# Kernel tuning notes

Hardware: AMD Instinct MI355X
Metric: run time of the kernel (lower is better)

The kernel has to match this reference:

```python
import jax, jax.numpy as jnp
import numpy as np

N_NODES = 100000
N_EDGES = 1600000
HID = 128
MAX_Z = 1000
N_GRAPHS = 1000
N_LAYERS = 3


def setup_inputs() -> dict:
    key = jax.random.key(0)
    ks = jax.random.split(key, 10)
    z = jax.random.randint(ks[0], (N_NODES,), 0, MAX_Z)
    edge_index = jax.random.randint(ks[1], (2, N_EDGES), 0, N_NODES)
    batch = jnp.sort(jax.random.randint(ks[2], (N_NODES,), 0, N_GRAPHS))
    s = 1.0 / np.sqrt(HID)
    z_emb = jax.random.normal(ks[3], (MAX_Z, HID), jnp.float32)
    Wl = jax.random.normal(ks[4], (N_LAYERS, HID, HID), jnp.float32) * s
    bl = jnp.zeros((N_LAYERS, HID), jnp.float32)
    Wr = jax.random.normal(ks[5], (N_LAYERS, HID, HID), jnp.float32) * s
    lin1_w = jax.random.normal(ks[6], (HID, HID), jnp.float32) * s
    lin1_b = jnp.zeros((HID,), jnp.float32)
    lin2_w = jax.random.normal(ks[7], (1, HID), jnp.float32) * s
    lin2_b = jnp.zeros((1,), jnp.float32)
    return dict(z=z, edge_index=edge_index, batch=batch, num_graphs=N_GRAPHS,
                z_emb=z_emb, Wl=Wl, bl=bl, Wr=Wr,
                lin1_w=lin1_w, lin1_b=lin1_b, lin2_w=lin2_w, lin2_b=lin2_b)


def _sage_conv(x, src, dst, deg_inv, Wl_i, bl_i, Wr_i):
    # PyG SAGEConv (default): out = lin_l(mean_{j in N(i)} x_j) + lin_r(x_i)
    agg = jax.ops.segment_sum(x[src], dst, num_segments=x.shape[0]) * deg_inv[:, None]
    return agg @ Wl_i.T + bl_i + x @ Wr_i.T


def reference(z, edge_index, batch, num_graphs, z_emb, Wl, bl, Wr, lin1_w, lin1_b, lin2_w, lin2_b):
    x = z_emb[z]  # z.ndim == 1 -> z_emb.ndim == 2, no sum branch
    src, dst = edge_index[0], edge_index[1]
    n = x.shape[0]
    deg = jax.ops.segment_sum(jnp.ones((src.shape[0],), x.dtype), dst, num_segments=n)
    deg_inv = 1.0 / jnp.maximum(deg, 1.0)  # mean aggregation; empty neighborhoods -> 0
    for i in range(Wl.shape[0] - 1):
        x = jax.nn.relu(_sage_conv(x, src, dst, deg_inv, Wl[i], bl[i], Wr[i]))
        # dropout is identity in eval mode
    x = _sage_conv(x, src, dst, deg_inv, Wl[-1], bl[-1], Wr[-1])
    # batch is sorted; first occurrence of each graph id == searchsorted
    center = jnp.searchsorted(batch, jnp.arange(num_graphs))
    h = x[center] * x[center + 1]
    h = jax.nn.relu(h @ lin1_w.T + lin1_b)
    return h @ lin2_w.T + lin2_b  # [num_graphs, 1]
```

## Files before the change

### kernel.cpp

```cpp
#include <hip/hip_runtime.h>
#include <hip/hip_bf16.h>
#include <cstdint>

#define HID 128
#define GM 128
#define SCAN_CHUNK 2048
#define NBIN 512
#define CHUNK 2048
#define MAXHI 1024

typedef __attribute__((ext_vector_type(8))) short bf16x8;
typedef __attribute__((ext_vector_type(4))) float f32x4;

__device__ __forceinline__ unsigned short f2bf(float f) {
    union { __hip_bfloat16 h; unsigned short u; } c;
    c.h = __float2bfloat16(f);
    return c.u;
}
__device__ __forceinline__ float bf2f(unsigned short u) {
    union { unsigned int i; float f; } c;
    c.i = ((unsigned int)u) << 16;
    return c.f;
}
__device__ __forceinline__ unsigned int pack2(unsigned short a, unsigned short b) {
    return (unsigned int)a | ((unsigned int)b << 16);
}
__device__ __forceinline__ bf16x8 ld_frag(const unsigned int* p) {
    union { uint4 u; bf16x8 f; } c;
    c.u = *(const uint4*)p;
    return c.f;
}

__device__ __forceinline__ int block_scan_excl(int v, int t, int* wtot, int* tot) {
    int lane = t & 63, wv = t >> 6;
    int incl = v;
#pragma unroll
    for (int off = 1; off < 64; off <<= 1) {
        int u = __shfl_up(incl, off);
        if (lane >= off) incl += u;
    }
    if (lane == 63) wtot[wv] = incl;
    __syncthreads();
    int woff = 0;
    for (int w = 0; w < wv; ++w) woff += wtot[w];
    if (tot) *tot = wtot[0] + wtot[1] + wtot[2] + wtot[3];
    __syncthreads();
    return woff + incl - v;
}

__global__ __launch_bounds__(256) void k_hist(const int* __restrict__ dst,
                                              int* __restrict__ hist, int n_edges) {
    __shared__ int h[NBIN];
    int t = threadIdx.x;
    h[t] = 0; h[t + 256] = 0;
    __syncthreads();
    int base = blockIdx.x * CHUNK;
#pragma unroll
    for (int j = 0; j < CHUNK / 256; ++j) {
        int e = base + j * 256 + t;
        if (e < n_edges) atomicAdd(&h[dst[e] & (NBIN - 1)], 1);
    }
    __syncthreads();
    hist[(size_t)blockIdx.x * NBIN + t] = h[t];
    hist[(size_t)blockIdx.x * NBIN + t + 256] = h[t + 256];
}

__global__ __launch_bounds__(256) void k_colscan(int* __restrict__ hist,
                                                 int* __restrict__ bintotal, int B) {
    __shared__ int wtot[4];
    int k = blockIdx.x, t = threadIdx.x;
    int run = 0;
    for (int base = 0; base < B; base += 256) {
        int b = base + t;
        int v = (b < B) ? hist[(size_t)b * NBIN + k] : 0;
        int tot;
        int excl = block_scan_excl(v, t, wtot, &tot);
        if (b < B) hist[(size_t)b * NBIN + k] = run + excl;
        run += tot;
    }
    if (t == 0) bintotal[k] = run;
}

__global__ __launch_bounds__(256) void k_binbase(const int* __restrict__ bintotal,
                                                 int* __restrict__ binbase) {
    __shared__ int wtot[4];
    int t = threadIdx.x;
    int a0 = bintotal[2 * t], a1 = bintotal[2 * t + 1];
    int excl = block_scan_excl(a0 + a1, t, wtot, nullptr);
    binbase[2 * t] = excl;
    binbase[2 * t + 1] = excl + a0;
    if (t == 255) binbase[NBIN] = excl + a0 + a1;
}

__global__ __launch_bounds__(256) void k_route(const int* __restrict__ src,
                                               const int* __restrict__ dst,
                                               const int* __restrict__ histex,
                                               const int* __restrict__ binbase,
                                               int2* __restrict__ ebuf, int n_edges) {
    __shared__ int h2[NBIN];
    __shared__ int basel[NBIN];
    int t = threadIdx.x;
    h2[t] = 0; h2[t + 256] = 0;
    basel[t]       = binbase[t]       + histex[(size_t)blockIdx.x * NBIN + t];
    basel[t + 256] = binbase[t + 256] + histex[(size_t)blockIdx.x * NBIN + t + 256];
    __syncthreads();
    int base = blockIdx.x * CHUNK;
#pragma unroll
    for (int j = 0; j < CHUNK / 256; ++j) {
        int e = base + j * 256 + t;
        if (e < n_edges) {
            int d = dst[e], s = src[e];
            int bin = d & (NBIN - 1);
            int r = atomicAdd(&h2[bin], 1);
            ebuf[basel[bin] + r] = make_int2(s, d);
        }
    }
}

__global__ __launch_bounds__(256) void k_group(const int2* __restrict__ ebuf,
                                               const int* __restrict__ binbase,
                                               const int* __restrict__ z,
                                               int* __restrict__ csr_src,
                                               int* __restrict__ csr_zoff,
                                               int* __restrict__ start, int* __restrict__ deg,
                                               int n_nodes) {
    __shared__ int hh[MAXHI];
    __shared__ int cur[MAXHI];
    __shared__ int wtot[4];
    int k = blockIdx.x, t = threadIdx.x;
    int rs = binbase[k], re = binbase[k + 1];
#pragma unroll
    for (int j = 0; j < MAXHI / 256; ++j) hh[t + j * 256] = 0;
    __syncthreads();
    for (int i = rs + t; i < re; i += 256)
        atomicAdd(&hh[ebuf[i].y >> 9], 1);
    __syncthreads();
    int idx = t * 4;
    int a0 = hh[idx], a1 = hh[idx + 1], a2 = hh[idx + 2], a3 = hh[idx + 3];
    int excl = block_scan_excl(a0 + a1 + a2 + a3, t, wtot, nullptr);
    int e0 = excl, e1 = e0 + a0, e2 = e1 + a1, e3 = e2 + a2;
    cur[idx] = e0; cur[idx + 1] = e1; cur[idx + 2] = e2; cur[idx + 3] = e3;
    int ee[4] = {e0, e1, e2, e3};
    int aa[4] = {a0, a1, a2, a3};
#pragma unroll
    for (int j = 0; j < 4; ++j) {
        int node = ((idx + j) << 9) | k;
        if (node < n_nodes) {
            start[node] = rs + ee[j];
            deg[node] = aa[j];
        }
    }
    __syncthreads();
    for (int i = rs + t; i < re; i += 256) {
        int2 sd = ebuf[i];
        int r = rs + atomicAdd(&cur[sd.y >> 9], 1);
        csr_src[r] = sd.x;
        csr_zoff[r] = z[sd.x] << 9;
    }
}

__global__ void k_scan1(const int* __restrict__ v_in, int* __restrict__ partials, int n) {
    __shared__ int sm[256];
    int t = threadIdx.x;
    int base = blockIdx.x * SCAN_CHUNK + t * 8;
    int s = 0;
#pragma unroll
    for (int j = 0; j < 8; ++j) { int i = base + j; if (i < n) s += v_in[i]; }
    sm[t] = s;
    __syncthreads();
    for (int off = 128; off > 0; off >>= 1) {
        if (t < off) sm[t] += sm[t + off];
        __syncthreads();
    }
    if (t == 0) partials[blockIdx.x] = sm[0];
}

__global__ void k_scan2(int* partials, int nchunks, int* total) {
    int lane = threadIdx.x;
    int v = (lane < nchunks) ? partials[lane] : 0;
#pragma unroll
    for (int off = 1; off < 64; off <<= 1) {
        int u = __shfl_up(v, off);
        if (lane >= off) v += u;
    }
    if (total && lane == nchunks - 1) *total = v;
    int ex = __shfl_up(v, 1);
    if (lane == 0) ex = 0;
    if (lane < nchunks) partials[lane] = ex;
}

__global__ void k_compact(const int* __restrict__ flag, const int* __restrict__ partials,
                          int* __restrict__ remap, int* __restrict__ nodes2, int n) {
    __shared__ int wtot[4];
    int t = threadIdx.x;
    int lane = t & 63, wv = t >> 6;
    int base = blockIdx.x * SCAN_CHUNK + t * 8;
    int v[8];
    int ts = 0;
#pragma unroll
    for (int j = 0; j < 8; ++j) { int i = base + j; v[j] = (i < n) ? flag[i] : 0; ts += v[j]; }
    int incl = ts;
#pragma unroll
    for (int off = 1; off < 64; off <<= 1) {
        int u = __shfl_up(incl, off);
        if (lane >= off) incl += u;
    }
    if (lane == 63) wtot[wv] = incl;
    __syncthreads();
    int woff = 0;
    for (int w = 0; w < wv; ++w) woff += wtot[w];
    int run = partials[blockIdx.x] + woff + (incl - ts);
#pragma unroll
    for (int j = 0; j < 8; ++j) {
        int i = base + j;
        if (i < n) {
            remap[i] = run;
            if (v[j]) nodes2[run] = i;
        }
        run += v[j];
    }
}

__global__ void k_prep(const float* __restrict__ z_emb, const float* __restrict__ Wl,
                       const float* __restrict__ Wr, const float* __restrict__ bl,
                       float* __restrict__ zl, float* __restrict__ zr,
                       unsigned short* __restrict__ wh, unsigned short* __restrict__ wlo,
                       int max_z) {
    int t = threadIdx.x;
    if ((int)blockIdx.x < max_z) {
        __shared__ float row[HID];
        int r = blockIdx.x;
        if (t < HID) row[t] = z_emb[(size_t)r * HID + t];
        __syncthreads();
        int d = t & 127;
        const float* w = (t < 128 ? Wl : Wr) + (size_t)d * HID;
        float acc = 0.f;
#pragma unroll
        for (int k4 = 0; k4 < HID / 4; ++k4) {
            float4 wv = *(const float4*)(w + k4 * 4);
            float4 hv = *(const float4*)&row[k4 * 4];
            acc += wv.x * hv.x + wv.y * hv.y + wv.z * hv.z + wv.w * hv.w;
        }
        if (t < 128) zl[(size_t)r * HID + d] = acc;
        else         zr[(size_t)r * HID + d] = acc + bl[d];
    } else {
        int idx = (blockIdx.x - max_z) * 256 + t;
        if (idx >= 3 * HID * 2 * HID) return;
        int l = idx / (HID * 2 * HID);
        int r = idx - l * (HID * 2 * HID);
        int d = r >> 8;
        int k = r & 255;
        float v = (k < HID) ? Wl[((size_t)l * HID + d) * HID + k]
                            : Wr[((size_t)l * HID + d) * HID + (k - HID)];
        unsigned short h = f2bf(v);
        unsigned short lo = f2bf(v - bf2f(h));
        wh[idx] = h;
        wlo[idx] = lo;
    }
}

__global__ void k_flag(const int* __restrict__ sel, const int* __restrict__ start,
                       const int* __restrict__ deg,
                       const int* __restrict__ csr_src, int* __restrict__ flag, int n_sel) {
    int r = (blockIdx.x * blockDim.x + threadIdx.x) >> 6;
    int lane = threadIdx.x & 63;
    if (r >= n_sel) return;
    int node = sel[r];
    if (lane == 0) flag[node] = 1;
    int s = start[node], e = s + deg[node];
    for (int i = s + lane; i < e; i += 64) flag[csr_src[i]] = 1;
}

template<int MODE>
__global__ __launch_bounds__(256) void k_agg(const float* __restrict__ xv_,
                      float* __restrict__ aggout,
                      const int* __restrict__ start, const int* __restrict__ deg,
                      const int* __restrict__ csr_src, const int* __restrict__ csr_zoff,
                      const int* __restrict__ idxmap, const int* __restrict__ remap,
                      const int* __restrict__ z, const float* __restrict__ zr,
                      int n_host, const int* __restrict__ n_dev) {
    int nw_total = gridDim.x * 4;
    int w0 = blockIdx.x * 4 + (threadIdx.x >> 6);
    int lane = threadIdx.x & 63;
    int n = n_dev ? *n_dev : n_host;
    int half = lane >> 5;
    int col = lane & 31;
    const float4* xv = (const float4*)xv_;
    const char* xc = (const char*)xv_;
    for (int r = w0; r < n; r += nw_total) {
        int node = (MODE == 1) ? r : idxmap[r];
        int s = start[node];
        int dg = deg[node];
        int e = s + dg;
        float4 a0 = {0.f,0.f,0.f,0.f};
        if (MODE == 1) {
            for (int i = s + half; i < e; i += 16) {
                int off[8];
                float msk[8];
#pragma unroll
                for (int k = 0; k < 8; ++k) {
                    int p = i + 2 * k;
                    bool valid = p < e;
                    off[k] = csr_zoff[valid ? p : e - 1];
                    msk[k] = valid ? 1.f : 0.f;
                }
                float4 v[8];
#pragma unroll
                for (int k = 0; k < 8; ++k)
                    v[k] = ((const float4*)(xc + off[k]))[col];
#pragma unroll
                for (int k = 0; k < 8; ++k) {
                    a0.x = fmaf(v[k].x, msk[k], a0.x);
                    a0.y = fmaf(v[k].y, msk[k], a0.y);
                    a0.z = fmaf(v[k].z, msk[k], a0.z);
                    a0.w = fmaf(v[k].w, msk[k], a0.w);
                }
            }
        } else {
            float4 a1 = {0.f,0.f,0.f,0.f}, a2 = {0.f,0.f,0.f,0.f}, a3 = {0.f,0.f,0.f,0.f};
            int i = s + half;
            for (; i + 6 < e; i += 8) {
                int s0 = csr_src[i];
                int s1 = csr_src[i + 2];
                int s2 = csr_src[i + 4];
                int s3 = csr_src[i + 6];
                if (MODE == 3) { s0 = remap[s0]; s1 = remap[s1]; s2 = remap[s2]; s3 = remap[s3]; }
                float4 v0 = xv[(size_t)s0 * 32 + col];
                float4 v1 = xv[(size_t)s1 * 32 + col];
                float4 v2 = xv[(size_t)s2 * 32 + col];
                float4 v3 = xv[(size_t)s3 * 32 + col];
                a0.x += v0.x; a0.y += v0.y; a0.z += v0.z; a0.w += v0.w;
                a1.x += v1.x; a1.y += v1.y; a1.z += v1.z; a1.w += v1.w;
                a2.x += v2.x; a2.y += v2.y; a2.z += v2.z; a2.w += v2.w;
                a3.x += v3.x; a3.y += v3.y; a3.z += v3.z; a3.w += v3.w;
            }
            for (; i < e; i += 2) {
                int s0 = csr_src[i];
                if (MODE == 3) s0 = remap[s0];
                float4 v0 = xv[(size_t)s0 * 32 + col];
                a0.x += v0.x; a0.y += v0.y; a0.z += v0.z; a0.w += v0.w;
            }
            a0.x += a1.x + a2.x + a3.x;
            a0.y += a1.y + a2.y + a3.y;
            a0.z += a1.z + a2.z + a3.z;
            a0.w += a1.w + a2.w + a3.w;
        }
        a0.x += __shfl_xor(a0.x, 32);
        a0.y += __shfl_xor(a0.y, 32);
        a0.z += __shfl_xor(a0.z, 32);
        a0.w += __shfl_xor(a0.w, 32);
        if (half == 0) {
            float di = 1.0f / fmaxf((float)dg, 1.0f);
            float4 o = make_float4(a0.x * di, a0.y * di, a0.z * di, a0.w * di);
            if (MODE == 1) {
                int zn = z[node];
                float4 rv = ((const float4*)zr)[(size_t)zn * 32 + col];
                o.x = fmaxf(o.x + rv.x, 0.f);
                o.y = fmaxf(o.y + rv.y, 0.f);
                o.z = fmaxf(o.z + rv.z, 0.f);
                o.w = fmaxf(o.w + rv.w, 0.f);
            }
            ((float4*)aggout)[(size_t)r * 32 + col] = o;
        }
    }
}

__global__ __launch_bounds__(256) void k_gemm(const float* __restrict__ aggsrc,
                                              const float* __restrict__ xsrc,
                                              float* __restrict__ out,
                                              const unsigned short* __restrict__ wh,
                                              const unsigned short* __restrict__ wlo,
                                              const float* __restrict__ bias,
                                              const int* __restrict__ xidx,
                                              const int* __restrict__ remap2,
                                              int n_host, const int* __restrict__ n_dev,
                                              int do_relu) {
    __shared__ unsigned int sAh[GM * 16], sAl[GM * 16];
    __shared__ unsigned int sBh[HID * 16], sBl[HID * 16];
    int n_rows = n_dev ? *n_dev : n_host;
    int t = threadIdx.x;
    int node0 = blockIdx.x * GM;
    if (node0 >= n_rows) return;
    int wv = t >> 6, lane = t & 63;
    int lrow = lane & 15, lk = lane >> 4;

    f32x4 acc[2][8];
#pragma unroll
    for (int m = 0; m < 2; ++m)
#pragma unroll
        for (int n = 0; n < 8; ++n) acc[m][n] = (f32x4){0.f, 0.f, 0.f, 0.f};

    int srow = t >> 2;
    int sq = t & 3;

    int gg[2] = {node0 + srow, node0 + srow + 64};
    bool vv[2] = {gg[0] < n_rows, gg[1] < n_rows};
    int xr[2];
#pragma unroll
    for (int rr = 0; rr < 2; ++rr) {
        int v = xidx ? (vv[rr] ? xidx[gg[rr]] : 0) : gg[rr];
        xr[rr] = remap2 ? remap2[v] : v;
    }

    for (int c = 0; c < 8; ++c) {
        int kbase = (c & 3) * 32;
        int kb = c * 32;
#pragma unroll
        for (int rr = 0; rr < 2; ++rr) {
            int row = srow + rr * 64;
            const float* srcrow = (c < 4) ? aggsrc + (size_t)gg[rr] * HID
                                          : xsrc + (size_t)xr[rr] * HID;
            float f[8];
            if (vv[rr]) {
                const float4* rp = (const float4*)(srcrow + kbase + sq * 8);
                float4 v0 = rp[0], v1 = rp[1];
                f[0]=v0.x; f[1]=v0.y; f[2]=v0.z; f[3]=v0.w;
                f[4]=v1.x; f[5]=v1.y; f[6]=v1.z; f[7]=v1.w;
            } else {
#pragma unroll
                for (int j = 0; j < 8; ++j) f[j] = 0.f;
            }
            unsigned int h[4], l[4];
#pragma unroll
            for (int j = 0; j < 4; ++j) {
                unsigned short h0 = f2bf(f[2*j]), h1 = f2bf(f[2*j+1]);
                unsigned short l0 = f2bf(f[2*j] - bf2f(h0));
                unsigned short l1 = f2bf(f[2*j+1] - bf2f(h1));
                h[j] = pack2(h0, h1);
                l[j] = pack2(l0, l1);
            }
            unsigned int base = row * 16 + sq * 4;
            *(uint4*)&sAh[base] = make_uint4(h[0], h[1], h[2], h[3]);
            *(uint4*)&sAl[base] = make_uint4(l[0], l[1], l[2], l[3]);
        }
#pragma unroll
        for (int rr = 0; rr < 2; ++rr) {
            int d = srow + rr * 64;
            size_t go = (size_t)d * 256 + kb + sq * 8;
            uint4 vh = *(const uint4*)(wh + go);
            uint4 vl = *(const uint4*)(wlo + go);
            unsigned int base = d * 16 + sq * 4;
            *(uint4*)&sBh[base] = vh;
            *(uint4*)&sBl[base] = vl;
        }
        __syncthreads();
        bf16x8 ah0, al0, ah1, al1;
        {
            unsigned int a0 = (unsigned)(wv * 32 + lrow) * 16 + lk * 4;
            unsigned int a1 = (unsigned)(wv * 32 + 16 + lrow) * 16 + lk * 4;
            ah0 = ld_frag(&sAh[a0]); al0 = ld_frag(&sAl[a0]);
            ah1 = ld_frag(&sAh[a1]); al1 = ld_frag(&sAl[a1]);
        }
#pragma unroll
        for (int n = 0; n < 8; ++n) {
            unsigned int b = (unsigned)(n * 16 + lrow) * 16 + lk * 4;
            bf16x8 bh = ld_frag(&sBh[b]);
            bf16x8 bl = ld_frag(&sBl[b]);
            acc[0][n] = __builtin_amdgcn_mfma_f32_16x16x32_bf16(ah0, bh, acc[0][n], 0, 0, 0);
            acc[0][n] = __builtin_amdgcn_mfma_f32_16x16x32_bf16(al0, bh, acc[0][n], 0, 0, 0);
            acc[0][n] = __builtin_amdgcn_mfma_f32_16x16x32_bf16(ah0, bl, acc[0][n], 0, 0, 0);
            acc[1][n] = __builtin_amdgcn_mfma_f32_16x16x32_bf16(ah1, bh, acc[1][n], 0, 0, 0);
            acc[1][n] = __builtin_amdgcn_mfma_f32_16x16x32_bf16(al1, bh, acc[1][n], 0, 0, 0);
            acc[1][n] = __builtin_amdgcn_mfma_f32_16x16x32_bf16(ah1, bl, acc[1][n], 0, 0, 0);
        }
        __syncthreads();
    }
#pragma unroll
    for (int m = 0; m < 2; ++m) {
        int rbase = node0 + wv * 32 + m * 16 + lk * 4;
#pragma unroll
        for (int n = 0; n < 8; ++n) {
            int colb = n * 16 + lrow;
            float bb = bias[colb];
#pragma unroll
            for (int r = 0; r < 4; ++r) {
                int row = rbase + r;
                if (row < n_rows) {
                    float v = acc[m][n][r] + bb;
                    if (do_relu) v = fmaxf(v, 0.f);
                    out[(size_t)row * HID + colb] = v;
                }
            }
        }
    }
}

__global__ void k_center(const int* __restrict__ batch, int* __restrict__ sel,
                         int n_nodes, int n_graphs) {
    int g = blockIdx.x * blockDim.x + threadIdx.x;
    if (g >= n_graphs) return;
    int lo = 0, hi = n_nodes;
    while (lo < hi) {
        int mid = (lo + hi) >> 1;
        if (batch[mid] < g) lo = mid + 1;
        else hi = mid;
    }
    sel[2 * g]     = min(lo, n_nodes - 1);
    sel[2 * g + 1] = min(lo + 1, n_nodes - 1);
}

__global__ void k_readout(const float* __restrict__ y,
                          const float* __restrict__ w1, const float* __restrict__ b1,
                          const float* __restrict__ w2, const float* __restrict__ b2,
                          float* __restrict__ out, int n_graphs) {
    __shared__ float h[HID];
    int g = blockIdx.x;
    if (g >= n_graphs) return;
    int lane = threadIdx.x;
    float2 a = ((const float2*)(y + (size_t)(2 * g) * HID))[lane];
    float2 b = ((const float2*)(y + (size_t)(2 * g + 1) * HID))[lane];
    h[2 * lane] = a.x * b.x;
    h[2 * lane + 1] = a.y * b.y;
    __syncthreads();
    int d0 = 2 * lane;
    float acc0 = b1[d0], acc1 = b1[d0 + 1];
    const float4* w1a = (const float4*)(w1 + (size_t)d0 * HID);
    const float4* w1b = (const float4*)(w1 + (size_t)(d0 + 1) * HID);
#pragma unroll 8
    for (int k4 = 0; k4 < HID / 4; ++k4) {
        float4 hv = *(const float4*)&h[k4 * 4];
        float4 wa = w1a[k4];
        float4 wb = w1b[k4];
        acc0 += hv.x * wa.x + hv.y * wa.y + hv.z * wa.z + hv.w * wa.w;
        acc1 += hv.x * wb.x + hv.y * wb.y + hv.z * wb.z + hv.w * wb.w;
    }
    float p = fmaxf(acc0, 0.f) * w2[d0] + fmaxf(acc1, 0.f) * w2[d0 + 1];
#pragma unroll
    for (int off = 32; off > 0; off >>= 1) p += __shfl_down(p, off);
    if (lane == 0) out[g] = p + b2[0];
}

extern "C" void kernel_launch(void* const* d_in, const int* in_sizes, int n_in,
                              void* d_out, int out_size, void* d_ws, size_t ws_size,
                              hipStream_t stream) {
    const int* z = (const int*)d_in[0];
    const int* edge_index = (const int*)d_in[1];
    const int* batch = (const int*)d_in[2];
    const float* z_emb = (const float*)d_in[4];
    const float* Wl = (const float*)d_in[5];
    const float* bl = (const float*)d_in[6];
    const float* Wr = (const float*)d_in[7];
    const float* lin1_w = (const float*)d_in[8];
    const float* lin1_b = (const float*)d_in[9];
    const float* lin2_w = (const float*)d_in[10];
    const float* lin2_b = (const float*)d_in[11];
    float* out = (float*)d_out;

    int n_nodes = in_sizes[0];
    int n_edges = in_sizes[1] / 2;
    int max_z = in_sizes[4] / HID;
    int n_graphs = out_size;
    int n_sel = 2 * n_graphs;

    const int* e_src = edge_index;
    const int* e_dst = edge_index + n_edges;

    char* p = (char*)d_ws;
    auto alloc = [&](size_t bytes) {
        char* r = p;
        p += (bytes + 511) & ~(size_t)511;
        return r;
    };
    float* x       = (float*)alloc((size_t)n_nodes * HID * 4);
    float* agg2    = (float*)alloc((size_t)n_nodes * HID * 4);
    float* x2c     = (float*)alloc((size_t)n_nodes * HID * 4);
    float* aggsel  = (float*)alloc((size_t)n_sel * HID * 4);
    float* y       = (float*)alloc((size_t)n_sel * HID * 4);
    int*   deg     = (int*)alloc((size_t)n_nodes * 4);
    int*   start   = (int*)alloc((size_t)n_nodes * 4);
    int2*  ebuf    = (int2*)alloc((size_t)n_edges * 8);
    int*   csr_src = (int*)alloc((size_t)n_edges * 4);
    int*   csr_zoff= (int*)alloc((size_t)n_edges * 4);
    int B = (n_edges + CHUNK - 1) / CHUNK;
    int*   hist     = (int*)alloc((size_t)B * NBIN * 4);
    int*   bintotal = (int*)alloc((size_t)NBIN * 4);
    int*   binbase  = (int*)alloc((size_t)(NBIN + 1) * 4);
    int*   parts  = (int*)alloc(64 * 4);
    int*   sel    = (int*)alloc((size_t)n_sel * 4);
    int*   flag   = (int*)alloc((size_t)n_nodes * 4);
    int*   remap  = (int*)alloc((size_t)n_nodes * 4);
    int*   nodes2 = (int*)alloc((size_t)n_nodes * 4);
    int*   n2     = (int*)alloc(4);
    float* zl     = (float*)alloc((size_t)max_z * HID * 4);
    float* zr     = (float*)alloc((size_t)max_z * HID * 4);
    unsigned short* wh  = (unsigned short*)alloc((size_t)3 * HID * 2 * HID * 2);
    unsigned short* wlo = (unsigned short*)alloc((size_t)3 * HID * 2 * HID * 2);

    hipMemsetAsync(flag, 0, (size_t)n_nodes * 4, stream);

    int wsplit_blocks = (3 * HID * 2 * HID + 255) / 256;
    k_prep<<<max_z + wsplit_blocks, 256, 0, stream>>>(z_emb, Wl, Wr, bl, zl, zr, wh, wlo, max_z);

    k_hist<<<B, 256, 0, stream>>>(e_dst, hist, n_edges);
    k_colscan<<<NBIN, 256, 0, stream>>>(hist, bintotal, B);
    k_binbase<<<1, 256, 0, stream>>>(bintotal, binbase);
    k_route<<<B, 256, 0, stream>>>(e_src, e_dst, hist, binbase, ebuf, n_edges);
    k_group<<<NBIN, 256, 0, stream>>>(ebuf, binbase, z, csr_src, csr_zoff, start, deg, n_nodes);

    k_center<<<(n_graphs + 255) / 256, 256, 0, stream>>>(batch, sel, n_nodes, n_graphs);

    k_flag<<<(n_sel * 64 + 255) / 256, 256, 0, stream>>>(sel, start, deg, csr_src, flag, n_sel);
    int nchunks = (n_nodes + SCAN_CHUNK - 1) / SCAN_CHUNK;
    k_scan1<<<nchunks, 256, 0, stream>>>(flag, parts, n_nodes);
    k_scan2<<<1, 64, 0, stream>>>(parts, nchunks, n2);
    k_compact<<<nchunks, 256, 0, stream>>>(flag, parts, remap, nodes2, n_nodes);

    int agg_blocks = (n_nodes + 3) / 4;
    k_agg<1><<<agg_blocks, 256, 0, stream>>>(zl, x, start, deg, csr_src, csr_zoff,
                                             nullptr, nullptr, z, zr, n_nodes, nullptr);
    k_agg<2><<<2048, 256, 0, stream>>>(x, agg2, start, deg, csr_src, nullptr, nodes2,
                                       nullptr, nullptr, nullptr, 0, n2);
    k_gemm<<<(n_nodes + GM - 1) / GM, 256, 0, stream>>>(agg2, x, x2c,
                                            wh + (size_t)HID * 2 * HID,
                                            wlo + (size_t)HID * 2 * HID,
                                            bl + HID, nodes2, nullptr, 0, n2, 1);
    k_agg<3><<<(n_sel + 3) / 4, 256, 0, stream>>>(x2c, aggsel, start, deg, csr_src, nullptr,
                                                  sel, remap, nullptr, nullptr, n_sel, nullptr);
    k_gemm<<<(n_sel + GM - 1) / GM, 256, 0, stream>>>(aggsel, x2c, y,
                                                      wh + (size_t)2 * HID * 2 * HID,
                                                      wlo + (size_t)2 * HID * 2 * HID,
                                                      bl + (size_t)2 * HID,
                                                      sel, remap, n_sel, nullptr, 0);
    k_readout<<<n_graphs, 64, 0, stream>>>(y, lin1_w, lin1_b, lin2_w, lin2_b, out, n_graphs);
}
```

Before: 263.6 us.

## Fuse preprocessing and tail kernels to cut launch count

Folds the bin-base scan into the column-scan kernel using a last-block-done counter. Merges center selection with neighbour flagging and replaces the three-pass compaction scan with a single wave-level scan plus one atomic per wave. The last-layer aggregate, GEMM and readout now run in one per-graph tail kernel using fp32 weights, and the MODE 1 aggregation gets a simpler unrolled loop with four accumulators. This removes several small launches and the memset. In exchange the compaction order becomes nondeterministic, and the tail kernel computes the GEMM with plain FMAs per graph.

After: 291.4 us. +10.5%, slower.

```diff
diff --git a/kernel.cpp b/kernel.cpp
--- a/kernel.cpp
+++ b/kernel.cpp
@@ -4,7 +4,6 @@
 
 #define HID 128
 #define GM 128
-#define SCAN_CHUNK 2048
 #define NBIN 512
 #define CHUNK 2048
 #define MAXHI 1024
@@ -48,186 +47,14 @@
     return woff + incl - v;
 }
 
-__global__ __launch_bounds__(256) void k_hist(const int* __restrict__ dst,
-                                              int* __restrict__ hist, int n_edges) {
-    __shared__ int h[NBIN];
-    int t = threadIdx.x;
-    h[t] = 0; h[t + 256] = 0;
-    __syncthreads();
-    int base = blockIdx.x * CHUNK;
-#pragma unroll
-    for (int j = 0; j < CHUNK / 256; ++j) {
-        int e = base + j * 256 + t;
-        if (e < n_edges) atomicAdd(&h[dst[e] & (NBIN - 1)], 1);
-    }
-    __syncthreads();
-    hist[(size_t)blockIdx.x * NBIN + t] = h[t];
-    hist[(size_t)blockIdx.x * NBIN + t + 256] = h[t + 256];
-}
-
-__global__ __launch_bounds__(256) void k_colscan(int* __restrict__ hist,
-                                                 int* __restrict__ bintotal, int B) {
-    __shared__ int wtot[4];
-    int k = blockIdx.x, t = threadIdx.x;
-    int run = 0;
-    for (int base = 0; base < B; base += 256) {
-        int b = base + t;
-        int v = (b < B) ? hist[(size_t)b * NBIN + k] : 0;
-        int tot;
-        int excl = block_scan_excl(v, t, wtot, &tot);
-        if (b < B) hist[(size_t)b * NBIN + k] = run + excl;
-        run += tot;
-    }
-    if (t == 0) bintotal[k] = run;
-}
-
-__global__ __launch_bounds__(256) void k_binbase(const int* __restrict__ bintotal,
-                                                 int* __restrict__ binbase) {
-    __shared__ int wtot[4];
-    int t = threadIdx.x;
-    int a0 = bintotal[2 * t], a1 = bintotal[2 * t + 1];
-    int excl = block_scan_excl(a0 + a1, t, wtot, nullptr);
-    binbase[2 * t] = excl;
-    binbase[2 * t + 1] = excl + a0;
-    if (t == 255) binbase[NBIN] = excl + a0 + a1;
-}
-
-__global__ __launch_bounds__(256) void k_route(const int* __restrict__ src,
-                                               const int* __restrict__ dst,
-                                               const int* __restrict__ histex,
-                                               const int* __restrict__ binbase,
-                                               int2* __restrict__ ebuf, int n_edges) {
-    __shared__ int h2[NBIN];
-    __shared__ int basel[NBIN];
-    int t = threadIdx.x;
-    h2[t] = 0; h2[t + 256] = 0;
-    basel[t]       = binbase[t]       + histex[(size_t)blockIdx.x * NBIN + t];
-    basel[t + 256] = binbase[t + 256] + histex[(size_t)blockIdx.x * NBIN + t + 256];
-    __syncthreads();
-    int base = blockIdx.x * CHUNK;
-#pragma unroll
-    for (int j = 0; j < CHUNK / 256; ++j) {
-        int e = base + j * 256 + t;
-        if (e < n_edges) {
-            int d = dst[e], s = src[e];
-            int bin = d & (NBIN - 1);
-            int r = atomicAdd(&h2[bin], 1);
-            ebuf[basel[bin] + r] = make_int2(s, d);
-        }
-    }
-}
-
-__global__ __launch_bounds__(256) void k_group(const int2* __restrict__ ebuf,
-                                               const int* __restrict__ binbase,
-                                               const int* __restrict__ z,
-                                               int* __restrict__ csr_src,
-                                               int* __restrict__ csr_zoff,
-                                               int* __restrict__ start, int* __restrict__ deg,
-                                               int n_nodes) {
-    __shared__ int hh[MAXHI];
-    __shared__ int cur[MAXHI];
-    __shared__ int wtot[4];
-    int k = blockIdx.x, t = threadIdx.x;
-    int rs = binbase[k], re = binbase[k + 1];
-#pragma unroll
-    for (int j = 0; j < MAXHI / 256; ++j) hh[t + j * 256] = 0;
-    __syncthreads();
-    for (int i = rs + t; i < re; i += 256)
-        atomicAdd(&hh[ebuf[i].y >> 9], 1);
-    __syncthreads();
-    int idx = t * 4;
-    int a0 = hh[idx], a1 = hh[idx + 1], a2 = hh[idx + 2], a3 = hh[idx + 3];
-    int excl = block_scan_excl(a0 + a1 + a2 + a3, t, wtot, nullptr);
-    int e0 = excl, e1 = e0 + a0, e2 = e1 + a1, e3 = e2 + a2;
-    cur[idx] = e0; cur[idx + 1] = e1; cur[idx + 2] = e2; cur[idx + 3] = e3;
-    int ee[4] = {e0, e1, e2, e3};
-    int aa[4] = {a0, a1, a2, a3};
-#pragma unroll
-    for (int j = 0; j < 4; ++j) {
-        int node = ((idx + j) << 9) | k;
-        if (node < n_nodes) {
-            start[node] = rs + ee[j];
-            deg[node] = aa[j];
-        }
-    }
-    __syncthreads();
-    for (int i = rs + t; i < re; i += 256) {
-        int2 sd = ebuf[i];
-        int r = rs + atomicAdd(&cur[sd.y >> 9], 1);
-        csr_src[r] = sd.x;
-        csr_zoff[r] = z[sd.x] << 9;
-    }
-}
-
-__global__ void k_scan1(const int* __restrict__ v_in, int* __restrict__ partials, int n) {
-    __shared__ int sm[256];
-    int t = threadIdx.x;
-    int base = blockIdx.x * SCAN_CHUNK + t * 8;
-    int s = 0;
-#pragma unroll
-    for (int j = 0; j < 8; ++j) { int i = base + j; if (i < n) s += v_in[i]; }
-    sm[t] = s;
-    __syncthreads();
-    for (int off = 128; off > 0; off >>= 1) {
-        if (t < off) sm[t] += sm[t + off];
-        __syncthreads();
-    }
-    if (t == 0) partials[blockIdx.x] = sm[0];
-}
-
-__global__ void k_scan2(int* partials, int nchunks, int* total) {
-    int lane = threadIdx.x;
-    int v = (lane < nchunks) ? partials[lane] : 0;
-#pragma unroll
-    for (int off = 1; off < 64; off <<= 1) {
-        int u = __shfl_up(v, off);
-        if (lane >= off) v += u;
-    }
-    if (total && lane == nchunks - 1) *total = v;
-    int ex = __shfl_up(v, 1);
-    if (lane == 0) ex = 0;
-    if (lane < nchunks) partials[lane] = ex;
-}
-
-__global__ void k_compact(const int* __restrict__ flag, const int* __restrict__ partials,
-                          int* __restrict__ remap, int* __restrict__ nodes2, int n) {
-    __shared__ int wtot[4];
-    int t = threadIdx.x;
-    int lane = t & 63, wv = t >> 6;
-    int base = blockIdx.x * SCAN_CHUNK + t * 8;
-    int v[8];
-    int ts = 0;
-#pragma unroll
-    for (int j = 0; j < 8; ++j) { int i = base + j; v[j] = (i < n) ? flag[i] : 0; ts += v[j]; }
-    int incl = ts;
-#pragma unroll
-    for (int off = 1; off < 64; off <<= 1) {
-        int u = __shfl_up(incl, off);
-        if (lane >= off) incl += u;
-    }
-    if (lane == 63) wtot[wv] = incl;
-    __syncthreads();
-    int woff = 0;
-    for (int w = 0; w < wv; ++w) woff += wtot[w];
-    int run = partials[blockIdx.x] + woff + (incl - ts);
-#pragma unroll
-    for (int j = 0; j < 8; ++j) {
-        int i = base + j;
-        if (i < n) {
-            remap[i] = run;
-            if (v[j]) nodes2[run] = i;
-        }
-        run += v[j];
-    }
-}
-
 __global__ void k_prep(const float* __restrict__ z_emb, const float* __restrict__ Wl,
                        const float* __restrict__ Wr, const float* __restrict__ bl,
                        float* __restrict__ zl, float* __restrict__ zr,
                        unsigned short* __restrict__ wh, unsigned short* __restrict__ wlo,
-                       int max_z) {
+                       int* __restrict__ done, int max_z) {
     int t = threadIdx.x;
     if ((int)blockIdx.x < max_z) {
+        if (blockIdx.x == 0 && t == 0) done[0] = 0;
         __shared__ float row[HID];
         int r = blockIdx.x;
         if (t < HID) row[t] = z_emb[(size_t)r * HID + t];
@@ -259,16 +86,167 @@
     }
 }
 
-__global__ void k_flag(const int* __restrict__ sel, const int* __restrict__ start,
-                       const int* __restrict__ deg,
-                       const int* __restrict__ csr_src, int* __restrict__ flag, int n_sel) {
-    int r = (blockIdx.x * blockDim.x + threadIdx.x) >> 6;
+__global__ __launch_bounds__(256) void k_hist(const int* __restrict__ dst,
+                                              int* __restrict__ hist, int n_edges) {
+    __shared__ int h[NBIN];
+    int t = threadIdx.x;
+    h[t] = 0; h[t + 256] = 0;
+    __syncthreads();
+    int base = blockIdx.x * CHUNK;
+#pragma unroll
+    for (int j = 0; j < CHUNK / 256; ++j) {
+        int e = base + j * 256 + t;
+        if (e < n_edges) atomicAdd(&h[dst[e] & (NBIN - 1)], 1);
+    }
+    __syncthreads();
+    hist[(size_t)blockIdx.x * NBIN + t] = h[t];
+    hist[(size_t)blockIdx.x * NBIN + t + 256] = h[t + 256];
+}
+
+__global__ __launch_bounds__(256) void k_colscan(int* __restrict__ hist,
+                                                 int* __restrict__ bintotal,
+                                                 int* __restrict__ binbase,
+                                                 int* __restrict__ done, int B) {
+    __shared__ int wtot[4];
+    __shared__ int slast;
+    int k = blockIdx.x, t = threadIdx.x;
+    int run = 0;
+    for (int base = 0; base < B; base += 256) {
+        int b = base + t;
+        int v = (b < B) ? hist[(size_t)b * NBIN + k] : 0;
+        int tot;
+        int excl = block_scan_excl(v, t, wtot, &tot);
+        if (b < B) hist[(size_t)b * NBIN + k] = run + excl;
+        run += tot;
+    }
+    if (t == 0) {
+        atomicExch(&bintotal[k], run);
+        __threadfence();
+        slast = (atomicAdd(done, 1) == NBIN - 1) ? 1 : 0;
+    }
+    __syncthreads();
+    if (!slast) return;
+    __threadfence();
+    int a0 = atomicAdd(&bintotal[2 * t], 0);
+    int a1 = atomicAdd(&bintotal[2 * t + 1], 0);
+    int excl = block_scan_excl(a0 + a1, t, wtot, nullptr);
+    binbase[2 * t] = excl;
+    binbase[2 * t + 1] = excl + a0;
+    if (t == 255) binbase[NBIN] = excl + a0 + a1;
+}
+
+__global__ __launch_bounds__(256) void k_route(const int* __restrict__ src,
+                                               const int* __restrict__ dst,
+                                               const int* __restrict__ histex,
+                                               const int* __restrict__ binbase,
+                                               int2* __restrict__ ebuf, int n_edges) {
+    __shared__ int h2[NBIN];
+    __shared__ int basel[NBIN];
+    int t = threadIdx.x;
+    h2[t] = 0; h2[t + 256] = 0;
+    basel[t]       = binbase[t]       + histex[(size_t)blockIdx.x * NBIN + t];
+    basel[t + 256] = binbase[t + 256] + histex[(size_t)blockIdx.x * NBIN + t + 256];
+    __syncthreads();
+    int base = blockIdx.x * CHUNK;
+#pragma unroll
+    for (int j = 0; j < CHUNK / 256; ++j) {
+        int e = base + j * 256 + t;
+        if (e < n_edges) {
+            int d = dst[e], s = src[e];
+            int bin = d & (NBIN - 1);
+            int r = atomicAdd(&h2[bin], 1);
+            ebuf[basel[bin] + r] = make_int2(s, d);
+        }
+    }
+}
+
+__global__ __launch_bounds__(256) void k_group(const int2* __restrict__ ebuf,
+                                               const int* __restrict__ binbase,
+                                               const int* __restrict__ z,
+                                               int* __restrict__ csr_src,
+                                               int* __restrict__ csr_zoff,
+                                               int* __restrict__ start, int* __restrict__ deg,
+                                               int* __restrict__ flag, int* __restrict__ n2,
+                                               int n_nodes) {
+    __shared__ int hh[MAXHI];
+    __shared__ int cur[MAXHI];
+    __shared__ int wtot[4];
+    int k = blockIdx.x, t = threadIdx.x;
+    if (k == 0 && t == 0) n2[0] = 0;
+    int rs = binbase[k], re = binbase[k + 1];
+#pragma unroll
+    for (int j = 0; j < MAXHI / 256; ++j) hh[t + j * 256] = 0;
+    __syncthreads();
+    for (int i = rs + t; i < re; i += 256)
+        atomicAdd(&hh[ebuf[i].y >> 9], 1);
+    __syncthreads();
+    int idx = t * 4;
+    int a0 = hh[idx], a1 = hh[idx + 1], a2 = hh[idx + 2], a3 = hh[idx + 3];
+    int excl = block_scan_excl(a0 + a1 + a2 + a3, t, wtot, nullptr);
+    int e0 = excl, e1 = e0 + a0, e2 = e1 + a1, e3 = e2 + a2;
+    cur[idx] = e0; cur[idx + 1] = e1; cur[idx + 2] = e2; cur[idx + 3] = e3;
+    int ee[4] = {e0, e1, e2, e3};
+    int aa[4] = {a0, a1, a2, a3};
+#pragma unroll
+    for (int j = 0; j < 4; ++j) {
+        int node = ((idx + j) << 9) | k;
+        if (node < n_nodes) {
+            start[node] = rs + ee[j];
+            deg[node] = aa[j];
+            flag[node] = 0;
+        }
+    }
+    __syncthreads();
+    for (int i = rs + t; i < re; i += 256) {
+        int2 sd = ebuf[i];
+        int r = rs + atomicAdd(&cur[sd.y >> 9], 1);
+        csr_src[r] = sd.x;
+        csr_zoff[r] = z[sd.x] << 9;
+    }
+}
+
+__global__ void k_centerflag(const int* __restrict__ batch, const int* __restrict__ start,
+                             const int* __restrict__ deg, const int* __restrict__ csr_src,
+                             int* __restrict__ sel, int* __restrict__ flag,
+                             int n_nodes, int n_graphs) {
+    int g = blockIdx.x;
+    if (g >= n_graphs) return;
+    int lane = threadIdx.x;
+    int lo = 0, hi = n_nodes;
+    while (lo < hi) {
+        int mid = (lo + hi) >> 1;
+        if (batch[mid] < g) lo = mid + 1;
+        else hi = mid;
+    }
+    int s0 = min(lo, n_nodes - 1);
+    int s1 = min(lo + 1, n_nodes - 1);
+    if (lane == 0) { sel[2 * g] = s0; sel[2 * g + 1] = s1; flag[s0] = 1; flag[s1] = 1; }
+    int a = start[s0], e = a + deg[s0];
+    for (int i = a + lane; i < e; i += 64) flag[csr_src[i]] = 1;
+    a = start[s1]; e = a + deg[s1];
+    for (int i = a + lane; i < e; i += 64) flag[csr_src[i]] = 1;
+}
+
+__global__ void k_flagcount(const int* __restrict__ flag, int* __restrict__ remap,
+                            int* __restrict__ nodes2, int* __restrict__ n2, int n) {
+    int i = blockIdx.x * blockDim.x + threadIdx.x;
     int lane = threadIdx.x & 63;
-    if (r >= n_sel) return;
-    int node = sel[r];
-    if (lane == 0) flag[node] = 1;
-    int s = start[node], e = s + deg[node];
-    for (int i = s + lane; i < e; i += 64) flag[csr_src[i]] = 1;
+    int f = (i < n) ? flag[i] : 0;
+    int incl = f;
+#pragma unroll
+    for (int off = 1; off < 64; off <<= 1) {
+        int u = __shfl_up(incl, off);
+        if (lane >= off) incl += u;
+    }
+    int wsum = __shfl(incl, 63);
+    int base = 0;
+    if (lane == 63) base = atomicAdd(n2, wsum);
+    base = __shfl(base, 63);
+    int pos = base + incl - f;
+    if (i < n) {
+        remap[i] = pos;
+        if (f) nodes2[pos] = i;
+    }
 }
 
 template<int MODE>
@@ -276,7 +254,7 @@
                       float* __restrict__ aggout,
                       const int* __restrict__ start, const int* __restrict__ deg,
                       const int* __restrict__ csr_src, const int* __restrict__ csr_zoff,
-                      const int* __restrict__ idxmap, const int* __restrict__ remap,
+                      const int* __restrict__ idxmap,
                       const int* __restrict__ z, const float* __restrict__ zr,
                       int n_host, const int* __restrict__ n_dev) {
     int nw_total = gridDim.x * 4;
@@ -292,39 +270,34 @@
         int s = start[node];
         int dg = deg[node];
         int e = s + dg;
-        float4 a0 = {0.f,0.f,0.f,0.f};
+        float4 a0 = {0.f,0.f,0.f,0.f}, a1 = {0.f,0.f,0.f,0.f};
+        float4 a2 = {0.f,0.f,0.f,0.f}, a3 = {0.f,0.f,0.f,0.f};
+        int i = s + half;
         if (MODE == 1) {
-            for (int i = s + half; i < e; i += 16) {
-                int off[8];
-                float msk[8];
-#pragma unroll
-                for (int k = 0; k < 8; ++k) {
-                    int p = i + 2 * k;
-                    bool valid = p < e;
-                    off[k] = csr_zoff[valid ? p : e - 1];
-                    msk[k] = valid ? 1.f : 0.f;
-                }
-                float4 v[8];
-#pragma unroll
-                for (int k = 0; k < 8; ++k)
-                    v[k] = ((const float4*)(xc + off[k]))[col];
-#pragma unroll
-                for (int k = 0; k < 8; ++k) {
-                    a0.x = fmaf(v[k].x, msk[k], a0.x);
-                    a0.y = fmaf(v[k].y, msk[k], a0.y);
-                    a0.z = fmaf(v[k].z, msk[k], a0.z);
-                    a0.w = fmaf(v[k].w, msk[k], a0.w);
-                }
+            for (; i + 6 < e; i += 8) {
+                int o0 = csr_zoff[i];
+                int o1 = csr_zoff[i + 2];
+                int o2 = csr_zoff[i + 4];
+                int o3 = csr_zoff[i + 6];
+                float4 v0 = *(const float4*)(xc + o0 + col * 16);
+                float4 v1 = *(const float4*)(xc + o1 + col * 16);
+                float4 v2 = *(const float4*)(xc + o2 + col * 16);
+                float4 v3 = *(const float4*)(xc + o3 + col * 16);
+                a0.x += v0.x; a0.y += v0.y; a0.z += v0.z; a0.w += v0.w;
+                a1.x += v1.x; a1.y += v1.y; a1.z += v1.z; a1.w += v1.w;
+                a2.x += v2.x; a2.y += v2.y; a2.z += v2.z; a2.w += v2.w;
+                a3.x += v3.x; a3.y += v3.y; a3.z += v3.z; a3.w += v3.w;
+            }
+            for (; i < e; i += 2) {
+                float4 v0 = *(const float4*)(xc + csr_zoff[i] + col * 16);
+                a0.x += v0.x; a0.y += v0.y; a0.z += v0.z; a0.w += v0.w;
             }
         } else {
-            float4 a1 = {0.f,0.f,0.f,0.f}, a2 = {0.f,0.f,0.f,0.f}, a3 = {0.f,0.f,0.f,0.f};
-            int i = s + half;
             for (; i + 6 < e; i += 8) {
                 int s0 = csr_src[i];
                 int s1 = csr_src[i + 2];
                 int s2 = csr_src[i + 4];
                 int s3 = csr_src[i + 6];
-                if (MODE == 3) { s0 = remap[s0]; s1 = remap[s1]; s2 = remap[s2]; s3 = remap[s3]; }
                 float4 v0 = xv[(size_t)s0 * 32 + col];
                 float4 v1 = xv[(size_t)s1 * 32 + col];
                 float4 v2 = xv[(size_t)s2 * 32 + col];
@@ -335,16 +308,14 @@
                 a3.x += v3.x; a3.y += v3.y; a3.z += v3.z; a3.w += v3.w;
             }
             for (; i < e; i += 2) {
-                int s0 = csr_src[i];
-                if (MODE == 3) s0 = remap[s0];
-                float4 v0 = xv[(size_t)s0 * 32 + col];
+                float4 v0 = xv[(size_t)csr_src[i] * 32 + col];
                 a0.x += v0.x; a0.y += v0.y; a0.z += v0.z; a0.w += v0.w;
             }
-            a0.x += a1.x + a2.x + a3.x;
-            a0.y += a1.y + a2.y + a3.y;
-            a0.z += a1.z + a2.z + a3.z;
-            a0.w += a1.w + a2.w + a3.w;
-        }
+        }
+        a0.x += a1.x + a2.x + a3.x;
+        a0.y += a1.y + a2.y + a3.y;
+        a0.z += a1.z + a2.z + a3.z;
+        a0.w += a1.w + a2.w + a3.w;
         a0.x += __shfl_xor(a0.x, 32);
         a0.y += __shfl_xor(a0.y, 32);
         a0.z += __shfl_xor(a0.z, 32);
@@ -372,7 +343,6 @@
                                               const unsigned short* __restrict__ wlo,
                                               const float* __restrict__ bias,
                                               const int* __restrict__ xidx,
-                                              const int* __restrict__ remap2,
                                               int n_host, const int* __restrict__ n_dev,
                                               int do_relu) {
     __shared__ unsigned int sAh[GM * 16], sAl[GM * 16];
@@ -397,10 +367,8 @@
     bool vv[2] = {gg[0] < n_rows, gg[1] < n_rows};
     int xr[2];
 #pragma unroll
-    for (int rr = 0; rr < 2; ++rr) {
-        int v = xidx ? (vv[rr] ? xidx[gg[rr]] : 0) : gg[rr];
-        xr[rr] = remap2 ? remap2[v] : v;
-    }
+    for (int rr = 0; rr < 2; ++rr)
+        xr[rr] = xidx ? (vv[rr] ? xidx[gg[rr]] : 0) : gg[rr];
 
     for (int c = 0; c < 8; ++c) {
         int kbase = (c & 3) * 32;
@@ -485,49 +453,89 @@
     }
 }
 
-__global__ void k_center(const int* __restrict__ batch, int* __restrict__ sel,
-                         int n_nodes, int n_graphs) {
-    int g = blockIdx.x * blockDim.x + threadIdx.x;
-    if (g >= n_graphs) return;
-    int lo = 0, hi = n_nodes;
-    while (lo < hi) {
-        int mid = (lo + hi) >> 1;
-        if (batch[mid] < g) lo = mid + 1;
-        else hi = mid;
-    }
-    sel[2 * g]     = min(lo, n_nodes - 1);
-    sel[2 * g + 1] = min(lo + 1, n_nodes - 1);
-}
-
-__global__ void k_readout(const float* __restrict__ y,
-                          const float* __restrict__ w1, const float* __restrict__ b1,
-                          const float* __restrict__ w2, const float* __restrict__ b2,
-                          float* __restrict__ out, int n_graphs) {
-    __shared__ float h[HID];
+__global__ __launch_bounds__(256) void k_tail(const float* __restrict__ x2c,
+                                              const int* __restrict__ sel,
+                                              const int* __restrict__ remap,
+                                              const int* __restrict__ start,
+                                              const int* __restrict__ deg,
+                                              const int* __restrict__ csr_src,
+                                              const float* __restrict__ Wl3,
+                                              const float* __restrict__ Wr3,
+                                              const float* __restrict__ b3,
+                                              const float* __restrict__ w1,
+                                              const float* __restrict__ b1,
+                                              const float* __restrict__ w2,
+                                              const float* __restrict__ b2,
+                                              float* __restrict__ out, int n_graphs) {
     int g = blockIdx.x;
     if (g >= n_graphs) return;
-    int lane = threadIdx.x;
-    float2 a = ((const float2*)(y + (size_t)(2 * g) * HID))[lane];
-    float2 b = ((const float2*)(y + (size_t)(2 * g + 1) * HID))[lane];
-    h[2 * lane] = a.x * b.x;
-    h[2 * lane + 1] = a.y * b.y;
-    __syncthreads();
-    int d0 = 2 * lane;
-    float acc0 = b1[d0], acc1 = b1[d0 + 1];
-    const float4* w1a = (const float4*)(w1 + (size_t)d0 * HID);
-    const float4* w1b = (const float4*)(w1 + (size_t)(d0 + 1) * HID);
+    __shared__ float sagg[2][HID];
+    __shared__ float sxs[2][HID];
+    __shared__ float stmp[2][HID];
+    __shared__ float sy[2][HID];
+    __shared__ float sh[HID];
+    __shared__ float sh2[HID];
+    int t = threadIdx.x;
+    int wv = t >> 6, lane = t & 63;
+    int r = wv >> 1;
+    int par = wv & 1;
+    int node = sel[2 * g + r];
+    int s = start[node], dgr = deg[node], e = s + dgr;
+    float2 acc = {0.f, 0.f};
+    for (int i = s + par; i < e; i += 2) {
+        int sr = remap[csr_src[i]];
+        float2 v = ((const float2*)x2c)[(size_t)sr * 64 + lane];
+        acc.x += v.x; acc.y += v.y;
+    }
+    if (par == 1) { stmp[r][2 * lane] = acc.x; stmp[r][2 * lane + 1] = acc.y; }
+    __syncthreads();
+    if (par == 0) {
+        float di = 1.0f / fmaxf((float)dgr, 1.0f);
+        sagg[r][2 * lane]     = (acc.x + stmp[r][2 * lane]) * di;
+        sagg[r][2 * lane + 1] = (acc.y + stmp[r][2 * lane + 1]) * di;
+        int xr = remap[node];
+        float2 xv = ((const float2*)x2c)[(size_t)xr * 64 + lane];
+        sxs[r][2 * lane] = xv.x; sxs[r][2 * lane + 1] = xv.y;
+    }
+    __syncthreads();
+    {
+        int r2 = t >> 7;
+        int d = t & 127;
+        const float4* wl = (const float4*)(Wl3 + (size_t)d * HID);
+        const float4* wr = (const float4*)(Wr3 + (size_t)d * HID);
+        float a = 0.f;
 #pragma unroll 8
-    for (int k4 = 0; k4 < HID / 4; ++k4) {
-        float4 hv = *(const float4*)&h[k4 * 4];
-        float4 wa = w1a[k4];
-        float4 wb = w1b[k4];
-        acc0 += hv.x * wa.x + hv.y * wa.y + hv.z * wa.z + hv.w * wa.w;
-        acc1 += hv.x * wb.x + hv.y * wb.y + hv.z * wb.z + hv.w * wb.w;
-    }
-    float p = fmaxf(acc0, 0.f) * w2[d0] + fmaxf(acc1, 0.f) * w2[d0 + 1];
-#pragma unroll
-    for (int off = 32; off > 0; off >>= 1) p += __shfl_down(p, off);
-    if (lane == 0) out[g] = p + b2[0];
+        for (int k4 = 0; k4 < HID / 4; ++k4) {
+            float4 w = wl[k4];
+            float4 v = *(const float4*)&sagg[r2][k4 * 4];
+            a += w.x * v.x + w.y * v.y + w.z * v.z + w.w * v.w;
+            float4 w2v = wr[k4];
+            float4 x = *(const float4*)&sxs[r2][k4 * 4];
+            a += w2v.x * x.x + w2v.y * x.y + w2v.z * x.z + w2v.w * x.w;
+        }
+        sy[r2][d] = a + b3[d];
+    }
+    __syncthreads();
+    if (t < HID) sh[t] = sy[0][t] * sy[1][t];
+    __syncthreads();
+    if (t < HID) {
+        const float4* wr1 = (const float4*)(w1 + (size_t)t * HID);
+        float a = b1[t];
+#pragma unroll 8
+        for (int k4 = 0; k4 < HID / 4; ++k4) {
+            float4 w = wr1[k4];
+            float4 h = *(const float4*)&sh[k4 * 4];
+            a += w.x * h.x + w.y * h.y + w.z * h.z + w.w * h.w;
+        }
+        sh2[t] = fmaxf(a, 0.f) * w2[t];
+    }
+    __syncthreads();
+    if (wv == 0) {
+        float p = sh2[lane] + sh2[lane + 64];
+#pragma unroll
+        for (int off = 32; off > 0; off >>= 1) p += __shfl_down(p, off);
+        if (lane == 0) out[g] = p + b2[0];
+    }
 }
 
 extern "C" void kernel_launch(void* const* d_in, const int* in_sizes, int n_in,
@@ -550,7 +558,6 @@
     int n_edges = in_sizes[1] / 2;
     int max_z = in_sizes[4] / HID;
     int n_graphs = out_size;
-    int n_sel = 2 * n_graphs;
 
     const int* e_src = edge_index;
     const int* e_dst = edge_index + n_edges;
@@ -564,8 +571,6 @@
     float* x       = (float*)alloc((size_t)n_nodes * HID * 4);
     float* agg2    = (float*)alloc((size_t)n_nodes * HID * 4);
     float* x2c     = (float*)alloc((size_t)n_nodes * HID * 4);
-    float* aggsel  = (float*)alloc((size_t)n_sel * HID * 4);
-    float* y       = (float*)alloc((size_t)n_sel * HID * 4);
     int*   deg     = (int*)alloc((size_t)n_nodes * 4);
     int*   start   = (int*)alloc((size_t)n_nodes * 4);
     int2*  ebuf    = (int2*)alloc((size_t)n_edges * 8);
@@ -575,8 +580,8 @@
     int*   hist     = (int*)alloc((size_t)B * NBIN * 4);
     int*   bintotal = (int*)alloc((size_t)NBIN * 4);
     int*   binbase  = (int*)alloc((size_t)(NBIN + 1) * 4);
-    int*   parts  = (int*)alloc(64 * 4);
-    int*   sel    = (int*)alloc((size_t)n_sel * 4);
+    int*   done     = (int*)alloc(4);
+    int*   sel    = (int*)alloc((size_t)(2 * n_graphs) * 4);
     int*   flag   = (int*)alloc((size_t)n_nodes * 4);
     int*   remap  = (int*)alloc((size_t)n_nodes * 4);
     int*   nodes2 = (int*)alloc((size_t)n_nodes * 4);
@@ -586,40 +591,33 @@
     unsigned short* wh  = (unsigned short*)alloc((size_t)3 * HID * 2 * HID * 2);
     unsigned short* wlo = (unsigned short*)alloc((size_t)3 * HID * 2 * HID * 2);
 
-    hipMemsetAsync(flag, 0, (size_t)n_nodes * 4, stream);
-
     int wsplit_blocks = (3 * HID * 2 * HID + 255) / 256;
-    k_prep<<<max_z + wsplit_blocks, 256, 0, stream>>>(z_emb, Wl, Wr, bl, zl, zr, wh, wlo, max_z);
+    k_prep<<<max_z + wsplit_blocks, 256, 0, stream>>>(z_emb, Wl, Wr, bl, zl, zr,
+                                                      wh, wlo, done, max_z);
 
     k_hist<<<B, 256, 0, stream>>>(e_dst, hist, n_edges);
-    k_colscan<<<NBIN, 256, 0, stream>>>(hist, bintotal, B);
-    k_binbase<<<1, 256, 0, stream>>>(bintotal, binbase);
+    k_colscan<<<NBIN, 256, 0, stream>>>(hist, bintotal, binbase, done, B);
     k_route<<<B, 256, 0, stream>>>(e_src, e_dst, hist, binbase, ebuf, n_edges);
-    k_group<<<NBIN, 256, 0, stream>>>(ebuf, binbase, z, csr_src, csr_zoff, start, deg, n_nodes);
-
-    k_center<<<(n_graphs + 255) / 256, 256, 0, stream>>>(batch, sel, n_nodes, n_graphs);
-
-    k_flag<<<(n_sel * 64 + 255) / 256, 256, 0, stream>>>(sel, start, deg, csr_src, flag, n_sel);
-    int nchunks = (n_nodes + SCAN_CHUNK - 1) / SCAN_CHUNK;
-    k_scan1<<<nchunks, 256, 0, stream>>>(flag, parts, n_nodes);
-    k_scan2<<<1, 64, 0, stream>>>(parts, nchunks, n2);
-    k_compact<<<nchunks, 256, 0, stream>>>(flag, parts, remap, nodes2, n_nodes);
+    k_group<<<NBIN, 256, 0, stream>>>(ebuf, binbase, z, csr_src, csr_zoff,
+                                      start, deg, flag, n2, n_nodes);
+
+    k_centerflag<<<n_graphs, 64, 0, stream>>>(batch, start, deg, csr_src, sel, flag,
+                                              n_nodes, n_graphs);
+    k_flagcount<<<(n_nodes + 255) / 256, 256, 0, stream>>>(flag, remap, nodes2, n2, n_nodes);
 
     int agg_blocks = (n_nodes + 3) / 4;
     k_agg<1><<<agg_blocks, 256, 0, stream>>>(zl, x, start, deg, csr_src, csr_zoff,
-                                             nullptr, nullptr, z, zr, n_nodes, nullptr);
+                                             nullptr, z, zr, n_nodes, nullptr);
     k_agg<2><<<2048, 256, 0, stream>>>(x, agg2, start, deg, csr_src, nullptr, nodes2,
-                                       nullptr, nullptr, nullptr, 0, n2);
+                                       nullptr, nullptr, 0, n2);
     k_gemm<<<(n_nodes + GM - 1) / GM, 256, 0, stream>>>(agg2, x, x2c,
                                             wh + (size_t)HID * 2 * HID,
                                             wlo + (size_t)HID * 2 * HID,
-                                            bl + HID, nodes2, nullptr, 0, n2, 1);
-    k_agg<3><<<(n_sel + 3) / 4, 256, 0, stream>>>(x2c, aggsel, start, deg, csr_src, nullptr,
-                                                  sel, remap, nullptr, nullptr, n_sel, nullptr);
-    k_gemm<<<(n_sel + GM - 1) / GM, 256, 0, stream>>>(aggsel, x2c, y,
-                                                      wh + (size_t)2 * HID * 2 * HID,
-                                                      wlo + (size_t)2 * HID * 2 * HID,
-                                                      bl + (size_t)2 * HID,
-                                                      sel, remap, n_sel, nullptr, 0);
-    k_readout<<<n_graphs, 64, 0, stream>>>(y, lin1_w, lin1_b, lin2_w, lin2_b, out, n_graphs);
-}
+                                            bl + HID, nodes2, 0, n2, 1);
+    k_tail<<<n_graphs, 256, 0, stream>>>(x2c, sel, remap, start, deg, csr_src,
+                                         Wl + (size_t)2 * HID * HID,
+                                         Wr + (size_t)2 * HID * HID,
+                                         bl + (size_t)2 * HID,
+                                         lin1_w, lin1_b, lin2_w, lin2_b,
+                                         out, n_graphs);
+}
```
